# Performance work log

Hardware: AMD Instinct MI355X
Metric: run time of the kernel (lower is better)

The kernel has to match this reference:

```python
import jax, jax.numpy as jnp
import numpy as np

IN_F = 4096
OUT_F = 4096
TOKENS = 8192
NNZ_PER_ROW = 64
NNZ = OUT_F * NNZ_PER_ROW
ALPHA = 1.0  # kill-switch default (full intelligence)


def setup_inputs() -> dict:
    key = jax.random.key(0)
    k1, k2, k3, k4, k5 = jax.random.split(key, 5)
    x = jax.random.normal(k1, (TOKENS, IN_F), dtype=jnp.float32)
    # nibble-packed int4 weights: each uint8 holds two int4 values (low|high<<4)
    base_weight = jax.random.randint(k2, (OUT_F, IN_F // 2), 0, 256, dtype=jnp.int32)
    # per-output-row dequant scales (fp16 in the module; fp32 math here)
    base_scales = jax.random.uniform(k3, (OUT_F,), dtype=jnp.float32) * 0.01 + 1e-4
    ortho_values = jax.random.normal(k4, (NNZ,), dtype=jnp.float32) * 0.02
    ortho_col_indices = jax.random.randint(k5, (NNZ,), 0, IN_F, dtype=jnp.int32)
    # CSR row pointer: exactly NNZ_PER_ROW nonzeros per output row
    ortho_row_ptr = (jnp.arange(OUT_F + 1, dtype=jnp.int32) * NNZ_PER_ROW)
    return {
        'x': x,
        'base_weight': base_weight,
        'base_scales': base_scales,
        'ortho_values': ortho_values,
        'ortho_col_indices': ortho_col_indices,
        'ortho_row_ptr': ortho_row_ptr,
    }


def _dequant_int4(base_weight, base_scales, in_f):
    # unpack nibbles: even flat index = low nibble, odd = high nibble (row-major)
    out_f = base_weight.shape[0]
    low = base_weight & 15
    high = (base_weight >> 4) & 15
    w = jnp.stack([low, high], axis=-1).reshape(out_f, in_f)  # [out, in] in 0..15
    w = jnp.where(w >= 8, w - 16, w)  # signed int4 in [-8, 7]
    return w.astype(base_scales.dtype) * base_scales[:, None]  # [out, in]


def _densify_csr(values, col_indices, row_ptr, out_f, in_f):
    nnz = values.shape[0]
    row_ids = jnp.searchsorted(row_ptr, jnp.arange(nnz, dtype=jnp.int32), side='right') - 1
    return jnp.zeros((out_f, in_f), values.dtype).at[row_ids, col_indices].add(values)


def reference(x, base_weight, base_scales, ortho_values, ortho_col_indices, ortho_row_ptr):
    out_f = base_weight.shape[0]
    in_f = x.shape[-1]
    W_base = _dequant_int4(base_weight, base_scales, in_f)          # [out, in]
    W_ortho = _densify_csr(ortho_values, ortho_col_indices, ortho_row_ptr, out_f, in_f)
    # Y = X @ W_base^T + alpha * X @ W_ortho^T  (fused as a single GEMM)
    W = W_base + ALPHA * W_ortho
    return x @ W.T  # [tokens, out]
```

## Files before the change

### kernel.cpp

```cpp
#include <hip/hip_runtime.h>
#include <hip/hip_bf16.h>

#define TOKENS 8192
#define IN_F   4096
#define OUT_F  4096

#define BM 256
#define BN 256
#define KSTEP 128
#define NT (IN_F / KSTEP)

typedef int   i32x4  __attribute__((ext_vector_type(4)));

#define BARRIER() asm volatile("s_barrier" ::: "memory")
#define VMCNT4()  asm volatile("s_waitcnt vmcnt(4)" ::: "memory")
#define VMCNT2()  asm volatile("s_waitcnt vmcnt(2)" ::: "memory")
#define VMCNT0()  asm volatile("s_waitcnt vmcnt(0)" ::: "memory")

__device__ __forceinline__ void gload_lds16(const void* g, void* l) {
  __builtin_amdgcn_global_load_lds(
      (const __attribute__((address_space(1))) void*)g,
      (__attribute__((address_space(3))) void*)l, 16, 0, 0);
}

__device__ __forceinline__ float blockmax256(float m, float* red) {
#pragma unroll
  for (int off = 32; off; off >>= 1)
    m = fmaxf(m, __shfl_xor(m, off, 64));
  if ((threadIdx.x & 63) == 0) red[threadIdx.x >> 6] = m;
  __syncthreads();
  return fmaxf(fmaxf(red[0], red[1]), fmaxf(red[2], red[3]));
}

__device__ __forceinline__ int pack4(const float* v, float inv) {
  unsigned w = 0;
#pragma unroll
  for (int b = 0; b < 4; ++b) {
    int q = __float2int_rn(fmaxf(fminf(v[b] * inv, 127.f), -127.f));
    w |= ((unsigned)(unsigned char)(signed char)q) << (8 * b);
  }
  return (int)w;
}

__global__ __launch_bounds__(256) void prep_w_i8(
    const int* __restrict__ bw, const float* __restrict__ scales,
    const float* __restrict__ vals, const int* __restrict__ cols,
    const int* __restrict__ rptr, signed char* __restrict__ Wq,
    float* __restrict__ sw) {
  __shared__ float row[IN_F];
  __shared__ float red[4];
  const int n = blockIdx.x;
  const int tid = threadIdx.x;
  const float s = scales[n];
  const int* bwr = bw + (size_t)n * (IN_F / 2);
#pragma unroll
  for (int it = 0; it < (IN_F / 2) / 256; ++it) {
    int j = it * 256 + tid;
    int p = bwr[j];
    int lo = p & 15;        lo = (lo >= 8) ? lo - 16 : lo;
    int hi = (p >> 4) & 15; hi = (hi >= 8) ? hi - 16 : hi;
    row[2 * j]     = (float)lo * s;
    row[2 * j + 1] = (float)hi * s;
  }
  __syncthreads();
  const int b = rptr[n], e = rptr[n + 1];
  for (int t = b + tid; t < e; t += 256)
    atomicAdd(&row[cols[t]], vals[t]);
  __syncthreads();
  float m = 0.f;
#pragma unroll
  for (int it = 0; it < IN_F / 256; ++it)
    m = fmaxf(m, fabsf(row[it * 256 + tid]));
  const float mm  = fmaxf(blockmax256(m, red), 1e-30f);
  const float inv = 127.f / mm;
  int4 w;
  w.x = pack4(&row[tid * 16 + 0],  inv);
  w.y = pack4(&row[tid * 16 + 4],  inv);
  w.z = pack4(&row[tid * 16 + 8],  inv);
  w.w = pack4(&row[tid * 16 + 12], inv);
  *(int4*)(Wq + (size_t)n * IN_F + tid * 16) = w;
  if (tid == 0) sw[n] = mm / 127.f;
}

__global__ __launch_bounds__(256) void cvt_x_i8(
    const float4* __restrict__ x, int* __restrict__ xq,
    float* __restrict__ sx) {
  __shared__ float red[4];
  const int tok = blockIdx.x;
  const int tid = threadIdx.x;
  const float4* xr = x + (size_t)tok * (IN_F / 4);
  float4 v[4];
  float m = 0.f;
#pragma unroll
  for (int j = 0; j < 4; ++j) {
    v[j] = xr[j * 256 + tid];
    m = fmaxf(m, fmaxf(fmaxf(fabsf(v[j].x), fabsf(v[j].y)),
                       fmaxf(fabsf(v[j].z), fabsf(v[j].w))));
  }
  const float mm  = fmaxf(blockmax256(m, red), 1e-30f);
  const float inv = 127.f / mm;
  int* xo = xq + (size_t)tok * (IN_F / 4);
#pragma unroll
  for (int j = 0; j < 4; ++j) {
    float vv[4] = {v[j].x, v[j].y, v[j].z, v[j].w};
    xo[j * 256 + tid] = pack4(vv, inv);
  }
  if (tid == 0) sx[tok] = mm / 127.f;
}

__global__ __launch_bounds__(512, 2) void gemm_i8(
    const unsigned char* __restrict__ A,
    const unsigned char* __restrict__ B,
    const float* __restrict__ sx,
    const float* __restrict__ sw,
    float* __restrict__ C) {
  __shared__ __align__(16) char lds[131072];

  const int nbn = OUT_F / BN;
  const int cpx = ((TOKENS / BM) * nbn) >> 3;
  const int bid = blockIdx.x;
  const int swz = (bid & 7) * cpx + (bid >> 3);
  const int tm = swz / nbn, tn = swz % nbn;
  const long m0 = (long)tm * BM;
  const long n0 = (long)tn * BN;

  const int tid  = threadIdx.x;
  const int lane = tid & 63;
  const int wid  = tid >> 6;
  const int wr   = wid >> 2;
  const int wc   = wid & 3;

  const int p0 = tid * 16;
  const int p1 = p0 + 8192;
  const int lin0 = p0 ^ (((p0 >> 9) & 1) << 5);
  const int lin1 = p1 ^ (((p1 >> 9) & 1) << 5);
  const int r0  = (((p0 >> 10) & 15) << 4) | ((lin0 >> 6) & 15);
  const int r1  = (((p1 >> 10) & 15) << 4) | ((lin1 >> 6) & 15);
  const int kb0 = lin0 & 63;
  const int kb1 = lin1 & 63;

  const unsigned char* Abase = A + m0 * IN_F;
  const unsigned char* Bbase = B + n0 * IN_F;

  int laneoff = ((lane & 15) << 6) | ((lane >> 4) << 4);
  laneoff ^= ((laneoff >> 9) & 1) << 5;

#define STAGE_A(nb, kt, h)                                                     \
  do {                                                                         \
    gload_lds16(Abase + (size_t)r0 * IN_F + (kt) * 128 + (h) * 64 + kb0,       \
                lds + (nb) * 65536 + (h) * 16384 + p0);                        \
    gload_lds16(Abase + (size_t)r1 * IN_F + (kt) * 128 + (h) * 64 + kb1,       \
                lds + (nb) * 65536 + (h) * 16384 + p1);                        \
  } while (0)
#define STAGE_B(nb, kt, h)                                                     \
  do {                                                                         \
    gload_lds16(Bbase + (size_t)r0 * IN_F + (kt) * 128 + (h) * 64 + kb0,       \
                lds + (nb) * 65536 + 32768 + (h) * 16384 + p0);                \
    gload_lds16(Bbase + (size_t)r1 * IN_F + (kt) * 128 + (h) * 64 + kb1,       \
                lds + (nb) * 65536 + 32768 + (h) * 16384 + p1);                \
  } while (0)

  i32x4 acc[8][4];
#pragma unroll
  for (int i = 0; i < 8; ++i)
#pragma unroll
    for (int j = 0; j < 4; ++j) acc[i][j] = (i32x4)0;

  i32x4 av1[4], av2[4], av3[4], av4[4], bv1[4], bv3[4];

  STAGE_A(0, 0, 0);
  STAGE_B(0, 0, 0);
  STAGE_A(0, 0, 1);
  STAGE_B(0, 0, 1);
  VMCNT4();
  BARRIER();
#pragma unroll
  for (int i = 0; i < 4; ++i)
    av1[i] = *(const i32x4*)(lds + (wr * 8 + i) * 1024 + laneoff);
#pragma unroll
  for (int j = 0; j < 4; ++j)
    bv1[j] = *(const i32x4*)(lds + 32768 + (wc * 4 + j) * 1024 + laneoff);

  for (int t = 0; t < NT; ++t) {
    const int b  = t & 1;
    const int nb = b ^ 1;
    const char* bufA  = lds + b * 65536;
    const char* bufB  = bufA + 32768;
    const char* nbufA = lds + nb * 65536;
    const char* nbufB = nbufA + 32768;
    const bool pf = (t + 1 < NT);

    BARRIER();
    __builtin_amdgcn_s_setprio(1);
    if (pf) STAGE_A(nb, t + 1, 0);
#pragma unroll
    for (int i = 0; i < 4; ++i)
      av2[i] = *(const i32x4*)(bufA + (wr * 8 + 4 + i) * 1024 + laneoff);
#pragma unroll
    for (int i = 0; i < 4; ++i)
#pragma unroll
      for (int j = 0; j < 4; ++j)
        acc[i][j] = __builtin_amdgcn_mfma_i32_16x16x64_i8(av1[i], bv1[j], acc[i][j], 0, 0, 0);
    __builtin_amdgcn_s_setprio(0);

    if (pf) { VMCNT2(); } else { VMCNT0(); }
    BARRIER();
    __builtin_amdgcn_s_setprio(1);
    if (pf) STAGE_B(nb, t + 1, 0);
#pragma unroll
    for (int i = 0; i < 4; ++i)
      av3[i] = *(const i32x4*)(bufA + 16384 + (wr * 8 + i) * 1024 + laneoff);
#pragma unroll
    for (int j = 0; j < 4; ++j)
      bv3[j] = *(const i32x4*)(bufB + 16384 + (wc * 4 + j) * 1024 + laneoff);
#pragma unroll
    for (int i = 0; i < 4; ++i)
#pragma unroll
      for (int j = 0; j < 4; ++j)
        acc[4 + i][j] = __builtin_amdgcn_mfma_i32_16x16x64_i8(av2[i], bv1[j], acc[4 + i][j], 0, 0, 0);
    __builtin_amdgcn_s_setprio(0);

    BARRIER();
    __builtin_amdgcn_s_setprio(1);
    if (pf) STAGE_A(nb, t + 1, 1);
#pragma unroll
    for (int i = 0; i < 4; ++i)
      av4[i] = *(const i32x4*)(bufA + 16384 + (wr * 8 + 4 + i) * 1024 + laneoff);
#pragma unroll
    for (int i = 0; i < 4; ++i)
#pragma unroll
      for (int j = 0; j < 4; ++j)
        acc[i][j] = __builtin_amdgcn_mfma_i32_16x16x64_i8(av3[i], bv3[j], acc[i][j], 0, 0, 0);
    __builtin_amdgcn_s_setprio(0);

    if (pf) { VMCNT2(); } else { VMCNT0(); }
    BARRIER();
    __builtin_amdgcn_s_setprio(1);
    if (pf) {
      STAGE_B(nb, t + 1, 1);
#pragma unroll
      for (int i = 0; i < 4; ++i)
        av1[i] = *(const i32x4*)(nbufA + (wr * 8 + i) * 1024 + laneoff);
#pragma unroll
      for (int j = 0; j < 4; ++j)
        bv1[j] = *(const i32x4*)(nbufB + (wc * 4 + j) * 1024 + laneoff);
    }
#pragma unroll
    for (int i = 0; i < 4; ++i)
#pragma unroll
      for (int j = 0; j < 4; ++j)
        acc[4 + i][j] = __builtin_amdgcn_mfma_i32_16x16x64_i8(av4[i], bv3[j], acc[4 + i][j], 0, 0, 0);
    __builtin_amdgcn_s_setprio(0);
  }
#undef STAGE_A
#undef STAGE_B

  const int er = (lane >> 4) * 4;
  const int ec = lane & 15;
#pragma unroll
  for (int i = 0; i < 8; ++i) {
    long rbase = m0 + wr * 128 + i * 16 + er;
    float sxq[4];
#pragma unroll
    for (int q = 0; q < 4; ++q) sxq[q] = sx[rbase + q];
#pragma unroll
    for (int j = 0; j < 4; ++j) {
      long cbase = n0 + wc * 64 + j * 16 + ec;
      const float swc = sw[cbase];
#pragma unroll
      for (int q = 0; q < 4; ++q)
        C[(rbase + q) * OUT_F + cbase] = (float)acc[i][j][q] * sxq[q] * swc;
    }
  }
}

__global__ __launch_bounds__(256) void fallback_kernel(
    const float* __restrict__ x, const int* __restrict__ bw,
    const float* __restrict__ scales, const float* __restrict__ vals,
    const int* __restrict__ cols, const int* __restrict__ rptr,
    float* __restrict__ out) {
  const int oc  = blockIdx.x * 64 + (threadIdx.x & 63);
  const int tok = blockIdx.y * 4 + (threadIdx.x >> 6);
  const float s = scales[oc];
  const int* bwr = bw + (size_t)oc * (IN_F / 2);
  const float* xr = x + (size_t)tok * IN_F;
  float acc = 0.f;
  for (int j = 0; j < IN_F / 2; ++j) {
    int p = bwr[j];
    int lo = p & 15;        lo = (lo >= 8) ? lo - 16 : lo;
    int hi = (p >> 4) & 15; hi = (hi >= 8) ? hi - 16 : hi;
    acc += ((float)lo * s) * xr[2 * j] + ((float)hi * s) * xr[2 * j + 1];
  }
  const int b = rptr[oc], e = rptr[oc + 1];
  for (int t = b; t < e; ++t) acc += vals[t] * xr[cols[t]];
  out[(size_t)tok * OUT_F + oc] = acc;
}

extern "C" void kernel_launch(void* const* d_in, const int* in_sizes, int n_in,
                              void* d_out, int out_size, void* d_ws, size_t ws_size,
                              hipStream_t stream) {
  const float* x      = (const float*)d_in[0];
  const int*   bw     = (const int*)d_in[1];
  const float* scales = (const float*)d_in[2];
  const float* vals   = (const float*)d_in[3];
  const int*   cols   = (const int*)d_in[4];
  const int*   rptr   = (const int*)d_in[5];
  float* out = (float*)d_out;

  const size_t wq_off = 0;
  const size_t xq_off = (size_t)OUT_F * IN_F;
  const size_t sw_off = xq_off + (size_t)TOKENS * IN_F;
  const size_t sx_off = sw_off + 65536;
  const size_t need   = sx_off + 65536;

  if (ws_size >= need) {
    signed char* Wq = (signed char*)d_ws + wq_off;
    signed char* Xq = (signed char*)d_ws + xq_off;
    float* sw = (float*)((char*)d_ws + sw_off);
    float* sx = (float*)((char*)d_ws + sx_off);
    prep_w_i8<<<OUT_F, 256, 0, stream>>>(bw, scales, vals, cols, rptr, Wq, sw);
    cvt_x_i8<<<TOKENS, 256, 0, stream>>>((const float4*)x, (int*)Xq, sx);
    gemm_i8<<<(TOKENS / BM) * (OUT_F / BN), 512, 0, stream>>>(
        (const unsigned char*)Xq, (const unsigned char*)Wq, sx, sw, out);
  } else {
    dim3 grid(OUT_F / 64, TOKENS / 4);
    fallback_kernel<<<grid, 256, 0, stream>>>(x, bw, scales, vals, cols, rptr, out);
  }
}
```

Baseline: 183.5 us.

## Collapse four-phase K-loop into two half-K phases with full drains

Result: slower. 191.9 us (+4.6%).

```diff
diff --git a/kernel.cpp b/kernel.cpp
--- a/kernel.cpp
+++ b/kernel.cpp
@@ -14,7 +14,6 @@
 
 #define BARRIER() asm volatile("s_barrier" ::: "memory")
 #define VMCNT4()  asm volatile("s_waitcnt vmcnt(4)" ::: "memory")
-#define VMCNT2()  asm volatile("s_waitcnt vmcnt(2)" ::: "memory")
 #define VMCNT0()  asm volatile("s_waitcnt vmcnt(0)" ::: "memory")
 
 __device__ __forceinline__ void gload_lds16(const void* g, void* l) {
@@ -166,7 +165,7 @@
 #pragma unroll
     for (int j = 0; j < 4; ++j) acc[i][j] = (i32x4)0;
 
-  i32x4 av1[4], av2[4], av3[4], av4[4], bv1[4], bv3[4];
+  i32x4 av1[8], av2[8], bv1[4], bv2[4];
 
   STAGE_A(0, 0, 0);
   STAGE_B(0, 0, 0);
@@ -175,7 +174,7 @@
   VMCNT4();
   BARRIER();
 #pragma unroll
-  for (int i = 0; i < 4; ++i)
+  for (int i = 0; i < 8; ++i)
     av1[i] = *(const i32x4*)(lds + (wr * 8 + i) * 1024 + laneoff);
 #pragma unroll
   for (int j = 0; j < 4; ++j)
@@ -190,66 +189,41 @@
     const char* nbufB = nbufA + 32768;
     const bool pf = (t + 1 < NT);
 
+    VMCNT0();
     BARRIER();
     __builtin_amdgcn_s_setprio(1);
-    if (pf) STAGE_A(nb, t + 1, 0);
-#pragma unroll
-    for (int i = 0; i < 4; ++i)
-      av2[i] = *(const i32x4*)(bufA + (wr * 8 + 4 + i) * 1024 + laneoff);
-#pragma unroll
-    for (int i = 0; i < 4; ++i)
+    if (pf) { STAGE_A(nb, t + 1, 0); STAGE_B(nb, t + 1, 0); }
+#pragma unroll
+    for (int i = 0; i < 8; ++i)
+      av2[i] = *(const i32x4*)(bufA + 16384 + (wr * 8 + i) * 1024 + laneoff);
+#pragma unroll
+    for (int j = 0; j < 4; ++j)
+      bv2[j] = *(const i32x4*)(bufB + 16384 + (wc * 4 + j) * 1024 + laneoff);
+#pragma unroll
+    for (int i = 0; i < 8; ++i)
 #pragma unroll
       for (int j = 0; j < 4; ++j)
         acc[i][j] = __builtin_amdgcn_mfma_i32_16x16x64_i8(av1[i], bv1[j], acc[i][j], 0, 0, 0);
     __builtin_amdgcn_s_setprio(0);
 
-    if (pf) { VMCNT2(); } else { VMCNT0(); }
-    BARRIER();
-    __builtin_amdgcn_s_setprio(1);
-    if (pf) STAGE_B(nb, t + 1, 0);
-#pragma unroll
-    for (int i = 0; i < 4; ++i)
-      av3[i] = *(const i32x4*)(bufA + 16384 + (wr * 8 + i) * 1024 + laneoff);
-#pragma unroll
-    for (int j = 0; j < 4; ++j)
-      bv3[j] = *(const i32x4*)(bufB + 16384 + (wc * 4 + j) * 1024 + laneoff);
-#pragma unroll
-    for (int i = 0; i < 4; ++i)
-#pragma unroll
-      for (int j = 0; j < 4; ++j)
-        acc[4 + i][j] = __builtin_amdgcn_mfma_i32_16x16x64_i8(av2[i], bv1[j], acc[4 + i][j], 0, 0, 0);
-    __builtin_amdgcn_s_setprio(0);
-
-    BARRIER();
-    __builtin_amdgcn_s_setprio(1);
-    if (pf) STAGE_A(nb, t + 1, 1);
-#pragma unroll
-    for (int i = 0; i < 4; ++i)
-      av4[i] = *(const i32x4*)(bufA + 16384 + (wr * 8 + 4 + i) * 1024 + laneoff);
-#pragma unroll
-    for (int i = 0; i < 4; ++i)
-#pragma unroll
-      for (int j = 0; j < 4; ++j)
-        acc[i][j] = __builtin_amdgcn_mfma_i32_16x16x64_i8(av3[i], bv3[j], acc[i][j], 0, 0, 0);
-    __builtin_amdgcn_s_setprio(0);
-
-    if (pf) { VMCNT2(); } else { VMCNT0(); }
+    VMCNT0();
     BARRIER();
     __builtin_amdgcn_s_setprio(1);
     if (pf) {
+      STAGE_A(nb, t + 1, 1);
       STAGE_B(nb, t + 1, 1);
 #pragma unroll
-      for (int i = 0; i < 4; ++i)
+      for (int i = 0; i < 8; ++i)
         av1[i] = *(const i32x4*)(nbufA + (wr * 8 + i) * 1024 + laneoff);
 #pragma unroll
       for (int j = 0; j < 4; ++j)
         bv1[j] = *(const i32x4*)(nbufB + (wc * 4 + j) * 1024 + laneoff);
     }
 #pragma unroll
-    for (int i = 0; i < 4; ++i)
+    for (int i = 0; i < 8; ++i)
 #pragma unroll
       for (int j = 0; j < 4; ++j)
-        acc[4 + i][j] = __builtin_amdgcn_mfma_i32_16x16x64_i8(av4[i], bv3[j], acc[4 + i][j], 0, 0, 0);
+        acc[i][j] = __builtin_amdgcn_mfma_i32_16x16x64_i8(av2[i], bv2[j], acc[i][j], 0, 0, 0);
     __builtin_amdgcn_s_setprio(0);
   }
 #undef STAGE_A
```

## Issue all next-tile prefetches up front and use a single barrier per K-step

Applied to the files above, without the earlier changes.

New measurement: 192.9 us. 1.05x slower.

```diff
diff --git a/kernel.cpp b/kernel.cpp
--- a/kernel.cpp
+++ b/kernel.cpp
@@ -14,8 +14,10 @@
 
 #define BARRIER() asm volatile("s_barrier" ::: "memory")
 #define VMCNT4()  asm volatile("s_waitcnt vmcnt(4)" ::: "memory")
-#define VMCNT2()  asm volatile("s_waitcnt vmcnt(2)" ::: "memory")
 #define VMCNT0()  asm volatile("s_waitcnt vmcnt(0)" ::: "memory")
+
+#define SGB(mask, n) __builtin_amdgcn_sched_group_barrier((mask), (n), 0)
+#define M_VMEM 0x10
 
 __device__ __forceinline__ void gload_lds16(const void* g, void* l) {
   __builtin_amdgcn_global_load_lds(
@@ -172,30 +174,31 @@
   STAGE_B(0, 0, 0);
   STAGE_A(0, 0, 1);
   STAGE_B(0, 0, 1);
-  VMCNT4();
+  VMCNT0();
   BARRIER();
-#pragma unroll
-  for (int i = 0; i < 4; ++i)
-    av1[i] = *(const i32x4*)(lds + (wr * 8 + i) * 1024 + laneoff);
-#pragma unroll
-  for (int j = 0; j < 4; ++j)
-    bv1[j] = *(const i32x4*)(lds + 32768 + (wc * 4 + j) * 1024 + laneoff);
 
   for (int t = 0; t < NT; ++t) {
     const int b  = t & 1;
     const int nb = b ^ 1;
     const char* bufA  = lds + b * 65536;
     const char* bufB  = bufA + 32768;
-    const char* nbufA = lds + nb * 65536;
-    const char* nbufB = nbufA + 32768;
     const bool pf = (t + 1 < NT);
 
-    BARRIER();
+    if (pf) {
+      STAGE_A(nb, t + 1, 0);
+      STAGE_B(nb, t + 1, 0);
+      STAGE_A(nb, t + 1, 1);
+      STAGE_B(nb, t + 1, 1);
+      SGB(M_VMEM, 8);
+    }
+
+#pragma unroll
+    for (int i = 0; i < 4; ++i)
+      av1[i] = *(const i32x4*)(bufA + (wr * 8 + i) * 1024 + laneoff);
+#pragma unroll
+    for (int j = 0; j < 4; ++j)
+      bv1[j] = *(const i32x4*)(bufB + (wc * 4 + j) * 1024 + laneoff);
     __builtin_amdgcn_s_setprio(1);
-    if (pf) STAGE_A(nb, t + 1, 0);
-#pragma unroll
-    for (int i = 0; i < 4; ++i)
-      av2[i] = *(const i32x4*)(bufA + (wr * 8 + 4 + i) * 1024 + laneoff);
 #pragma unroll
     for (int i = 0; i < 4; ++i)
 #pragma unroll
@@ -203,16 +206,10 @@
         acc[i][j] = __builtin_amdgcn_mfma_i32_16x16x64_i8(av1[i], bv1[j], acc[i][j], 0, 0, 0);
     __builtin_amdgcn_s_setprio(0);
 
-    if (pf) { VMCNT2(); } else { VMCNT0(); }
-    BARRIER();
+#pragma unroll
+    for (int i = 0; i < 4; ++i)
+      av2[i] = *(const i32x4*)(bufA + (wr * 8 + 4 + i) * 1024 + laneoff);
     __builtin_amdgcn_s_setprio(1);
-    if (pf) STAGE_B(nb, t + 1, 0);
-#pragma unroll
-    for (int i = 0; i < 4; ++i)
-      av3[i] = *(const i32x4*)(bufA + 16384 + (wr * 8 + i) * 1024 + laneoff);
-#pragma unroll
-    for (int j = 0; j < 4; ++j)
-      bv3[j] = *(const i32x4*)(bufB + 16384 + (wc * 4 + j) * 1024 + laneoff);
 #pragma unroll
     for (int i = 0; i < 4; ++i)
 #pragma unroll
@@ -220,12 +217,13 @@
         acc[4 + i][j] = __builtin_amdgcn_mfma_i32_16x16x64_i8(av2[i], bv1[j], acc[4 + i][j], 0, 0, 0);
     __builtin_amdgcn_s_setprio(0);
 
-    BARRIER();
+#pragma unroll
+    for (int i = 0; i < 4; ++i)
+      av3[i] = *(const i32x4*)(bufA + 16384 + (wr * 8 + i) * 1024 + laneoff);
+#pragma unroll
+    for (int j = 0; j < 4; ++j)
+      bv3[j] = *(const i32x4*)(bufB + 16384 + (wc * 4 + j) * 1024 + laneoff);
     __builtin_amdgcn_s_setprio(1);
-    if (pf) STAGE_A(nb, t + 1, 1);
-#pragma unroll
-    for (int i = 0; i < 4; ++i)
-      av4[i] = *(const i32x4*)(bufA + 16384 + (wr * 8 + 4 + i) * 1024 + laneoff);
 #pragma unroll
     for (int i = 0; i < 4; ++i)
 #pragma unroll
@@ -233,24 +231,19 @@
         acc[i][j] = __builtin_amdgcn_mfma_i32_16x16x64_i8(av3[i], bv3[j], acc[i][j], 0, 0, 0);
     __builtin_amdgcn_s_setprio(0);
 
-    if (pf) { VMCNT2(); } else { VMCNT0(); }
-    BARRIER();
+#pragma unroll
+    for (int i = 0; i < 4; ++i)
+      av4[i] = *(const i32x4*)(bufA + 16384 + (wr * 8 + 4 + i) * 1024 + laneoff);
     __builtin_amdgcn_s_setprio(1);
-    if (pf) {
-      STAGE_B(nb, t + 1, 1);
-#pragma unroll
-      for (int i = 0; i < 4; ++i)
-        av1[i] = *(const i32x4*)(nbufA + (wr * 8 + i) * 1024 + laneoff);
-#pragma unroll
-      for (int j = 0; j < 4; ++j)
-        bv1[j] = *(const i32x4*)(nbufB + (wc * 4 + j) * 1024 + laneoff);
-    }
 #pragma unroll
     for (int i = 0; i < 4; ++i)
 #pragma unroll
       for (int j = 0; j < 4; ++j)
         acc[4 + i][j] = __builtin_amdgcn_mfma_i32_16x16x64_i8(av4[i], bv3[j], acc[4 + i][j], 0, 0, 0);
     __builtin_amdgcn_s_setprio(0);
+
+    VMCNT0();
+    BARRIER();
   }
 #undef STAGE_A
 #undef STAGE_B
```
